# Performance work log

Hardware: AMD Instinct MI355X
Metric: run time of the kernel (lower is better)

The kernel has to match this reference:

```python
import jax, jax.numpy as jnp
import numpy as np

B, C, T, H, Wd = 8, 256, 16, 28, 28

def setup_inputs() -> dict:
    key = jax.random.key(0)
    k1, k2 = jax.random.split(key)
    in_data = jax.random.normal(k1, (B, C, T, H, Wd), dtype=jnp.float32)
    # conv_whh weight [C, C, 1, 1, 1] squeezed to [C_out, C_in]; scaled like kaiming init
    W = jax.random.normal(k2, (C, C), dtype=jnp.float32) * (1.0 / jnp.sqrt(jnp.float32(C)))
    return {"in_data": in_data, "W": W}

def reference(in_data, W):
    # h_0 = x_0; h_t = (W @ h_{t-1} + x_t) / 2, out = stack over t
    x0 = in_data[:, :, 0]                      # [B, C, H, W]
    xs = jnp.moveaxis(in_data[:, :, 1:], 2, 0) # [T-1, B, C, H, W]

    def step(h, x_t):
        h_new = (jnp.einsum('oc,bchw->bohw', W, h) + x_t) * 0.5
        return h_new, h_new

    _, outs = jax.lax.scan(step, x0, xs)       # [T-1, B, C, H, W]
    out = jnp.concatenate([x0[None], outs], axis=0)  # [T, B, C, H, W]
    return jnp.moveaxis(out, 0, 2)             # [B, C, T, H, W]
```

## Files before the change

### kernel.cpp

```cpp
#include <hip/hip_runtime.h>


typedef __attribute__((ext_vector_type(8))) short bf16x8;
typedef __attribute__((ext_vector_type(4))) float f32x4;
typedef __attribute__((ext_vector_type(4))) short short4v;

#define NTILES 49
#define LDSK   264

__device__ __forceinline__ short f2bf(float f) {
    union { float f; unsigned u; } v; v.f = f;
    unsigned r = v.u + 0x7FFFu + ((v.u >> 16) & 1u);
    return (short)(r >> 16);
}

__global__ __launch_bounds__(256, 2)
void rcu_kernel(const float* __restrict__ in, const float* __restrict__ Wm,
                float* __restrict__ out) {
    __shared__ short hbuf[2][16][LDSK];

    const int tid  = threadIdx.x;
    const int wave = tid >> 6;
    const int lane = tid & 63;
    const int l15  = lane & 15;
    const int quad = lane >> 4;

    const int b  = blockIdx.x / NTILES;
    const int s0 = (blockIdx.x % NTILES) * 16;

    bf16x8 a_frag[4][8];
#pragma unroll
    for (int mt = 0; mt < 4; ++mt) {
        const int m = wave * 64 + mt * 16 + l15;
        const float* wrow = Wm + m * 256 + quad * 8;
#pragma unroll
        for (int ks = 0; ks < 8; ++ks) {
            float4 f0 = *(const float4*)(wrow + ks * 32);
            float4 f1 = *(const float4*)(wrow + ks * 32 + 4);
            bf16x8 a;
            a[0] = f2bf(f0.x); a[1] = f2bf(f0.y); a[2] = f2bf(f0.z); a[3] = f2bf(f0.w);
            a[4] = f2bf(f1.x); a[5] = f2bf(f1.y); a[6] = f2bf(f1.z); a[7] = f2bf(f1.w);
            a_frag[mt][ks] = a;
        }
    }

    const size_t base = (size_t)b * 256 * 16 * 784 + s0;
    const float* xin  = in  + base;
    float*       xout = out + base;

    {
        const int sg = tid & 15;
        const int cg = tid >> 4;
#pragma unroll
        for (int i = 0; i < 16; ++i) {
            const int c = cg * 16 + i;
            const size_t off = (size_t)c * 16 * 784 + sg;
            const float v = xin[off];
            xout[off] = v;
            hbuf[0][sg][c] = f2bf(v);
        }
    }
    __syncthreads();

    int cur = 0;
    for (int t = 1; t < 16; ++t) {
        bf16x8 bfrag[8];
        const short* hp = &hbuf[cur][l15][quad * 8];
#pragma unroll
        for (int ks = 0; ks < 8; ++ks)
            bfrag[ks] = *(const bf16x8*)(hp + ks * 32);

        const int nxt = cur ^ 1;
#pragma unroll
        for (int mt = 0; mt < 4; ++mt) {
            f32x4 acc = {0.f, 0.f, 0.f, 0.f};
#pragma unroll
            for (int ks = 0; ks < 8; ++ks)
                acc = __builtin_amdgcn_mfma_f32_16x16x32_bf16(a_frag[mt][ks], bfrag[ks], acc, 0, 0, 0);

            const int c0 = wave * 64 + mt * 16 + quad * 4;
            short4v hbf;
#pragma unroll
            for (int r = 0; r < 4; ++r) {
                const size_t off = ((size_t)(c0 + r) * 16 + t) * 784 + l15;
                const float v = 0.5f * (acc[r] + xin[off]);
                xout[off] = v;
                hbf[r] = f2bf(v);
            }
            *(short4v*)&hbuf[nxt][l15][c0] = hbf;
        }
        __syncthreads();
        cur = nxt;
    }
}

extern "C" void kernel_launch(void* const* d_in, const int* in_sizes, int n_in,
                              void* d_out, int out_size, void* d_ws, size_t ws_size,
                              hipStream_t stream) {
    const float* in  = (const float*)d_in[0];
    const float* Wm  = (const float*)d_in[1];
    float*       out = (float*)d_out;
    hipLaunchKernelGGL(rcu_kernel, dim3(8 * NTILES), dim3(256), 0, stream, in, Wm, out);
}
```

Measured before the change: 230.0 us.

## Prefetch next timestep inputs into registers and relax barrier wait

Each timestep's input values are loaded one step ahead into registers, so global-load latency overlaps the MFMA work of the current step instead of sitting on the recurrence's critical path. The time loop is fully unrolled. The barrier is replaced with inline asm that waits only on LDS counters, so outstanding global loads and stores are not drained at each step. Packed bf16 conversion uses the HIP intrinsic. In exchange, register pressure rises, which could cause spills under the 2-blocks launch bound.

```diff
diff --git a/kernel.cpp b/kernel.cpp
--- a/kernel.cpp
+++ b/kernel.cpp
@@ -1,12 +1,17 @@
 #include <hip/hip_runtime.h>
+#include <hip/hip_bf16.h>
 
 
 typedef __attribute__((ext_vector_type(8))) short bf16x8;
 typedef __attribute__((ext_vector_type(4))) float f32x4;
-typedef __attribute__((ext_vector_type(4))) short short4v;
 
 #define NTILES 49
 #define LDSK   264
+
+__device__ __forceinline__ int pkbf2(float a, float b) {
+    __hip_bfloat162 h = __float22bfloat162_rn(make_float2(a, b));
+    union { __hip_bfloat162 h2; int i; } u; u.h2 = h; return u.i;
+}
 
 __device__ __forceinline__ short f2bf(float f) {
     union { float f; unsigned u; } v; v.f = f;
@@ -48,27 +53,46 @@
     const float* xin  = in  + base;
     float*       xout = out + base;
 
-    {
-        const int sg = tid & 15;
-        const int cg = tid >> 4;
+    float px[16];
 #pragma unroll
-        for (int i = 0; i < 16; ++i) {
-            const int c = cg * 16 + i;
-            const size_t off = (size_t)c * 16 * 784 + sg;
-            const float v = xin[off];
-            xout[off] = v;
-            hbuf[0][sg][c] = f2bf(v);
+    for (int mt = 0; mt < 4; ++mt) {
+        const int c0 = wave * 64 + mt * 16 + quad * 4;
+        float v[4];
+#pragma unroll
+        for (int r = 0; r < 4; ++r) {
+            const size_t off = (size_t)(c0 + r) * 16 * 784 + l15;
+            v[r] = xin[off];
+            xout[off] = v[r];
         }
+        int2 packed;
+        packed.x = pkbf2(v[0], v[1]);
+        packed.y = pkbf2(v[2], v[3]);
+        *(int2*)&hbuf[0][l15][c0] = packed;
+#pragma unroll
+        for (int r = 0; r < 4; ++r)
+            px[mt * 4 + r] = xin[((size_t)(c0 + r) * 16 + 1) * 784 + l15];
     }
     __syncthreads();
 
     int cur = 0;
+#pragma unroll
     for (int t = 1; t < 16; ++t) {
         bf16x8 bfrag[8];
         const short* hp = &hbuf[cur][l15][quad * 8];
 #pragma unroll
         for (int ks = 0; ks < 8; ++ks)
             bfrag[ks] = *(const bf16x8*)(hp + ks * 32);
+
+        float pxn[16];
+        if (t < 15) {
+#pragma unroll
+            for (int mt = 0; mt < 4; ++mt) {
+                const int c0 = wave * 64 + mt * 16 + quad * 4;
+#pragma unroll
+                for (int r = 0; r < 4; ++r)
+                    pxn[mt * 4 + r] = xin[((size_t)(c0 + r) * 16 + (t + 1)) * 784 + l15];
+            }
+        }
 
         const int nxt = cur ^ 1;
 #pragma unroll
@@ -79,17 +103,22 @@
                 acc = __builtin_amdgcn_mfma_f32_16x16x32_bf16(a_frag[mt][ks], bfrag[ks], acc, 0, 0, 0);
 
             const int c0 = wave * 64 + mt * 16 + quad * 4;
-            short4v hbf;
+            float v[4];
 #pragma unroll
             for (int r = 0; r < 4; ++r) {
-                const size_t off = ((size_t)(c0 + r) * 16 + t) * 784 + l15;
-                const float v = 0.5f * (acc[r] + xin[off]);
-                xout[off] = v;
-                hbf[r] = f2bf(v);
+                v[r] = 0.5f * (acc[r] + px[mt * 4 + r]);
+                xout[((size_t)(c0 + r) * 16 + t) * 784 + l15] = v[r];
             }
-            *(short4v*)&hbuf[nxt][l15][c0] = hbf;
+            int2 packed;
+            packed.x = pkbf2(v[0], v[1]);
+            packed.y = pkbf2(v[2], v[3]);
+            *(int2*)&hbuf[nxt][l15][c0] = packed;
         }
-        __syncthreads();
+
+        __asm__ volatile("s_waitcnt lgkmcnt(0)\n\ts_barrier" ::: "memory");
+
+#pragma unroll
+        for (int i = 0; i < 16; ++i) px[i] = pxn[i];
         cur = nxt;
     }
 }
```

After: 303.0 us. +31.7%, slower.
